# Performance work log

Hardware: AMD Instinct MI355X
Metric: run time of the kernel (lower is better)

The kernel has to match this reference:

```python
import jax, jax.numpy as jnp
import numpy as np


def setup_inputs() -> dict:
    key = jax.random.key(0)
    k1, k2, k3, k4 = jax.random.split(key, 4)
    N, E, DIN, DOUT = 16384, 8192, 128, 128
    x = jax.random.normal(k1, (N, DIN), dtype=jnp.float32)
    # sparse binary incidence matrix, avg node degree ~ E * 0.005 ~ 41
    H = (jax.random.uniform(k2, (N, E)) < 0.005).astype(jnp.float32)
    W = jax.random.normal(k3, (DOUT, DIN), dtype=jnp.float32) * (1.0 / np.sqrt(DIN))
    b = jax.random.normal(k4, (DOUT,), dtype=jnp.float32) * 0.01
    return {"x": x, "H": H, "W": W, "b": b}


def reference(x, H, W, b):
    # Degree vectors. Original builds dense diag matrices; off-diagonal zeros
    # raised to negative powers become inf and are zeroed by nan_to_num, so the
    # math reduces to elementwise inverse powers of the degree vectors with
    # non-finite entries mapped to 0.
    deg_node = jnp.sum(H, axis=1)                    # [N]
    deg_edge = jnp.sum(H, axis=0)                    # [E]
    dvih = jnp.where(deg_node > 0, deg_node ** -0.5, 0.0)   # D_v^{-1/2}
    dei = jnp.where(deg_edge > 0, 1.0 / deg_edge, 0.0)      # D_e^{-1}
    # D_v^{-1/2} H D_e^{-1} H^T D_v^{-1/2} x, as broadcasted row scalings
    y = dvih[:, None] * x                            # [N, DIN]
    y = H.T @ y                                      # [E, DIN]
    y = dei[:, None] * y                             # [E, DIN]
    y = H @ y                                        # [N, DIN]
    y = dvih[:, None] * y                            # [N, DIN]
    return y @ W.T + b                               # [N, DOUT]
```

## Files before the change

### kernel.cpp

```cpp
#include <hip/hip_runtime.h>
#include <hip/hip_bf16.h>

#define NN 16384
#define EE 8192
#define DD 128
#define CSR_STRIDE 128
#define CSC_STRIDE 192

typedef float vfloat4 __attribute__((ext_vector_type(4)));

__device__ __forceinline__ unsigned short f2bf(float f) {
    union { float f; unsigned u; } c; c.f = f;
    unsigned u = c.u + (0x7FFFu + ((c.u >> 16) & 1u));
    return (unsigned short)(u >> 16);
}
__device__ __forceinline__ float bf2f(unsigned short h) {
    union { unsigned u; float f; } c; c.u = ((unsigned)h) << 16;
    return c.f;
}


__global__ __launch_bounds__(256) void g_gemm(
    const float* __restrict__ x,
    const float* __restrict__ W,
    ushort4* __restrict__ xwb,
    int* __restrict__ edge_cnt)
{
    const int t = threadIdx.x;
    {
        int tid = blockIdx.x * 256 + t;
        if (tid < EE) edge_cnt[tid] = 0;
    }

    __shared__ float sA[32 * 132];
    __shared__ float sW[64 * 132];
    const int m0 = blockIdx.x * 32;

#pragma unroll
    for (int r = 0; r < 4; ++r) {
        int i = t + 256 * r;
        int row = i >> 5, c4 = (i & 31) << 2;
        *(float4*)&sA[row * 132 + c4] =
            *(const float4*)&x[(size_t)(m0 + row) * DD + c4];
    }

    const int jg = t & 15;
    const int mg = t >> 4;
    const int m2 = mg * 2;
    const int j4 = jg * 4;

    for (int h = 0; h < 2; ++h) {
        __syncthreads();
#pragma unroll
        for (int r = 0; r < 8; ++r) {
            int i = t + 256 * r;
            int row = i >> 5, c4 = (i & 31) << 2;
            *(float4*)&sW[row * 132 + c4] =
                *(const float4*)&W[(size_t)(h * 64 + row) * DD + c4];
        }
        __syncthreads();

        float acc0[4] = {0.f, 0.f, 0.f, 0.f};
        float acc1[4] = {0.f, 0.f, 0.f, 0.f};
#pragma unroll 4
        for (int k = 0; k < 128; k += 4) {
            float4 a0 = *(const float4*)&sA[m2 * 132 + k];
            float4 a1 = *(const float4*)&sA[(m2 + 1) * 132 + k];
#pragma unroll
            for (int jj = 0; jj < 4; ++jj) {
                float4 w = *(const float4*)&sW[(j4 + jj) * 132 + k];
                acc0[jj] += a0.x*w.x + a0.y*w.y + a0.z*w.z + a0.w*w.w;
                acc1[jj] += a1.x*w.x + a1.y*w.y + a1.z*w.z + a1.w*w.w;
            }
        }
        ushort4 p0, p1;
        p0.x = f2bf(acc0[0]); p0.y = f2bf(acc0[1]); p0.z = f2bf(acc0[2]); p0.w = f2bf(acc0[3]);
        p1.x = f2bf(acc1[0]); p1.y = f2bf(acc1[1]); p1.z = f2bf(acc1[2]); p1.w = f2bf(acc1[3]);
        xwb[(size_t)(m0 + m2)     * 32 + h * 16 + jg] = p0;
        xwb[(size_t)(m0 + m2 + 1) * 32 + h * 16 + jg] = p1;
    }
}

__global__ __launch_bounds__(256) void k1_parse(
    const float* __restrict__ H,
    float* __restrict__ dvih,
    int* __restrict__ csr_cnt,
    int* __restrict__ csr_idx,
    int* __restrict__ edge_cnt,
    int* __restrict__ csc_idx)
{
    const int n = blockIdx.x;
    const int t = threadIdx.x;
    __shared__ int s_cnt;
    __shared__ int s_list[CSR_STRIDE];
    if (t == 0) s_cnt = 0;
    __syncthreads();

    const vfloat4* row = (const vfloat4*)(H + (size_t)n * EE);
#pragma unroll
    for (int j = 0; j < 8; ++j) {
        int idx = t + 256 * j;
        vfloat4 v = __builtin_nontemporal_load(row + idx);
        int base = idx * 4;
        if (v[0] != 0.0f) { int p = atomicAdd(&s_cnt, 1); if (p < CSR_STRIDE) s_list[p] = base + 0; }
        if (v[1] != 0.0f) { int p = atomicAdd(&s_cnt, 1); if (p < CSR_STRIDE) s_list[p] = base + 1; }
        if (v[2] != 0.0f) { int p = atomicAdd(&s_cnt, 1); if (p < CSR_STRIDE) s_list[p] = base + 2; }
        if (v[3] != 0.0f) { int p = atomicAdd(&s_cnt, 1); if (p < CSR_STRIDE) s_list[p] = base + 3; }
    }
    __syncthreads();

    int cnt = s_cnt; if (cnt > CSR_STRIDE) cnt = CSR_STRIDE;
    if (t < cnt) {
        int e = s_list[t];
        csr_idx[(size_t)n * CSR_STRIDE + t] = e;
        int pos = atomicAdd(&edge_cnt[e], 1);
        if (pos < CSC_STRIDE) csc_idx[(size_t)e * CSC_STRIDE + pos] = n;
    }
    if (t == 0) {
        csr_cnt[n] = cnt;
        dvih[n] = (cnt > 0) ? (1.0f / sqrtf((float)cnt)) : 0.0f;
    }
}

__global__ __launch_bounds__(256) void k2_edge_gather(
    const ushort4* __restrict__ xwb,
    const float* __restrict__ dvih,
    const int* __restrict__ edge_cnt,
    const int* __restrict__ csc_idx,
    ushort4* __restrict__ y2b)
{
    const int t    = threadIdx.x;
    const int w    = t >> 6;
    const int lane = t & 63;
    const int grp  = lane >> 5;
    const int fl   = lane & 31;
    const int e    = blockIdx.x * 4 + w;

    __shared__ int    s_lst[4][CSC_STRIDE];
    __shared__ float  s_dv[4][CSC_STRIDE];

    int cnt = edge_cnt[e];
    int ccnt = cnt > CSC_STRIDE ? CSC_STRIDE : cnt;
    for (int i = lane; i < ccnt; i += 64) {
        int n = csc_idx[(size_t)e * CSC_STRIDE + i];
        s_lst[w][i] = n;
        s_dv[w][i]  = dvih[n];
    }
    __syncthreads();

    float ax = 0.f, ay = 0.f, az = 0.f, aw = 0.f;
    int i = grp;
    for (; i + 14 < ccnt; i += 16) {
        ushort4 v0 = xwb[(size_t)s_lst[w][i     ] * 32 + fl];
        ushort4 v1 = xwb[(size_t)s_lst[w][i +  2] * 32 + fl];
        ushort4 v2 = xwb[(size_t)s_lst[w][i +  4] * 32 + fl];
        ushort4 v3 = xwb[(size_t)s_lst[w][i +  6] * 32 + fl];
        ushort4 v4 = xwb[(size_t)s_lst[w][i +  8] * 32 + fl];
        ushort4 v5 = xwb[(size_t)s_lst[w][i + 10] * 32 + fl];
        ushort4 v6 = xwb[(size_t)s_lst[w][i + 12] * 32 + fl];
        ushort4 v7 = xwb[(size_t)s_lst[w][i + 14] * 32 + fl];
        float f0 = s_dv[w][i],      f1 = s_dv[w][i +  2];
        float f2 = s_dv[w][i +  4], f3 = s_dv[w][i +  6];
        float f4 = s_dv[w][i +  8], f5 = s_dv[w][i + 10];
        float f6 = s_dv[w][i + 12], f7 = s_dv[w][i + 14];
        ax += f0*bf2f(v0.x) + f1*bf2f(v1.x) + f2*bf2f(v2.x) + f3*bf2f(v3.x)
            + f4*bf2f(v4.x) + f5*bf2f(v5.x) + f6*bf2f(v6.x) + f7*bf2f(v7.x);
        ay += f0*bf2f(v0.y) + f1*bf2f(v1.y) + f2*bf2f(v2.y) + f3*bf2f(v3.y)
            + f4*bf2f(v4.y) + f5*bf2f(v5.y) + f6*bf2f(v6.y) + f7*bf2f(v7.y);
        az += f0*bf2f(v0.z) + f1*bf2f(v1.z) + f2*bf2f(v2.z) + f3*bf2f(v3.z)
            + f4*bf2f(v4.z) + f5*bf2f(v5.z) + f6*bf2f(v6.z) + f7*bf2f(v7.z);
        aw += f0*bf2f(v0.w) + f1*bf2f(v1.w) + f2*bf2f(v2.w) + f3*bf2f(v3.w)
            + f4*bf2f(v4.w) + f5*bf2f(v5.w) + f6*bf2f(v6.w) + f7*bf2f(v7.w);
    }
    for (; i < ccnt; i += 2) {
        ushort4 v = xwb[(size_t)s_lst[w][i] * 32 + fl];
        float f = s_dv[w][i];
        ax += f*bf2f(v.x); ay += f*bf2f(v.y); az += f*bf2f(v.z); aw += f*bf2f(v.w);
    }

    ax += __shfl_xor(ax, 32);
    ay += __shfl_xor(ay, 32);
    az += __shfl_xor(az, 32);
    aw += __shfl_xor(aw, 32);

    if (grp == 0) {
        float dei = (cnt > 0) ? (1.0f / (float)cnt) : 0.0f;
        ushort4 o;
        o.x = f2bf(ax * dei);
        o.y = f2bf(ay * dei);
        o.z = f2bf(az * dei);
        o.w = f2bf(aw * dei);
        y2b[(size_t)e * 32 + fl] = o;
    }
}

__global__ __launch_bounds__(256) void k3_node_gather(
    const ushort4* __restrict__ y2b,
    const float* __restrict__ dvih,
    const int* __restrict__ csr_cnt,
    const int* __restrict__ csr_idx,
    const float* __restrict__ b,
    float* __restrict__ out)
{
    const int t    = threadIdx.x;
    const int w    = t >> 6;
    const int lane = t & 63;
    const int grp  = lane >> 5;
    const int fl   = lane & 31;
    const int n    = blockIdx.x * 4 + w;

    __shared__ int s_lst[4][CSR_STRIDE];

    int cnt = csr_cnt[n];
    for (int i = lane; i < cnt; i += 64)
        s_lst[w][i] = csr_idx[(size_t)n * CSR_STRIDE + i];
    __syncthreads();

    float ax = 0.f, ay = 0.f, az = 0.f, aw = 0.f;
    int i = grp;
    for (; i + 6 < cnt; i += 8) {
        ushort4 v0 = y2b[(size_t)s_lst[w][i    ] * 32 + fl];
        ushort4 v1 = y2b[(size_t)s_lst[w][i + 2] * 32 + fl];
        ushort4 v2 = y2b[(size_t)s_lst[w][i + 4] * 32 + fl];
        ushort4 v3 = y2b[(size_t)s_lst[w][i + 6] * 32 + fl];
        ax += bf2f(v0.x) + bf2f(v1.x) + bf2f(v2.x) + bf2f(v3.x);
        ay += bf2f(v0.y) + bf2f(v1.y) + bf2f(v2.y) + bf2f(v3.y);
        az += bf2f(v0.z) + bf2f(v1.z) + bf2f(v2.z) + bf2f(v3.z);
        aw += bf2f(v0.w) + bf2f(v1.w) + bf2f(v2.w) + bf2f(v3.w);
    }
    for (; i < cnt; i += 2) {
        ushort4 v = y2b[(size_t)s_lst[w][i] * 32 + fl];
        ax += bf2f(v.x); ay += bf2f(v.y); az += bf2f(v.z); aw += bf2f(v.w);
    }

    ax += __shfl_xor(ax, 32);
    ay += __shfl_xor(ay, 32);
    az += __shfl_xor(az, 32);
    aw += __shfl_xor(aw, 32);

    if (grp == 0) {
        float dv = dvih[n];
        float4 bb = ((const float4*)b)[fl];
        float4 o = make_float4(ax * dv + bb.x,
                               ay * dv + bb.y,
                               az * dv + bb.z,
                               aw * dv + bb.w);
        ((float4*)out)[(size_t)n * 32 + fl] = o;
    }
}

extern "C" void kernel_launch(void* const* d_in, const int* in_sizes, int n_in,
                              void* d_out, int out_size, void* d_ws, size_t ws_size,
                              hipStream_t stream) {
    const float* x = (const float*)d_in[0];
    const float* H = (const float*)d_in[1];
    const float* W = (const float*)d_in[2];
    const float* b = (const float*)d_in[3];
    float* out = (float*)d_out;

    char* ws = (char*)d_ws;
    float*   dvih    = (float*)  (ws + 0);
    int*     csr_cnt = (int*)    (ws + 65536);
    int*     edge_cnt= (int*)    (ws + 131072);
    int*     csr_idx = (int*)    (ws + 163840);
    int*     csc_idx = (int*)    (ws + 8552448);
    ushort4* xwb     = (ushort4*)(ws + 14843904);
    ushort4* y2b     = (ushort4*)(ws + 19038208);

    g_gemm<<<NN / 32, 256, 0, stream>>>(x, W, xwb, edge_cnt);
    k1_parse<<<NN, 256, 0, stream>>>(H, dvih, csr_cnt, csr_idx, edge_cnt, csc_idx);
    k2_edge_gather<<<EE / 4, 256, 0, stream>>>(xwb, dvih, edge_cnt, csc_idx, y2b);
    k3_node_gather<<<NN / 4, 256, 0, stream>>>(y2b, dvih, csr_cnt, csr_idx, b, out);
}
```

Before: 729.9 us.

## Fuse GEMM and H-parse into one launch, move edge_cnt reset to memset

Merges the dense x·W^T GEMM and the H-row parse into a single kernel, with the first 512 blocks doing the GEMM and the rest parsing H rows, so the small GEMM overlaps with the bandwidth-bound H scan. The GEMM now reads x and W directly from global memory with no LDS staging. The edge_cnt zeroing moves to a hipMemsetAsync, and the index loads in the gather kernels become nontemporal. The trade-off is more global and L2 traffic in the GEMM blocks and an extra memset launch.

```diff
diff --git a/kernel.cpp b/kernel.cpp
--- a/kernel.cpp
+++ b/kernel.cpp
@@ -6,6 +6,7 @@
 #define DD 128
 #define CSR_STRIDE 128
 #define CSC_STRIDE 192
+#define GEMM_BLOCKS 512
 
 typedef float vfloat4 __attribute__((ext_vector_type(4)));
 
@@ -20,79 +21,55 @@
 }
 
 
-__global__ __launch_bounds__(256) void g_gemm(
+__global__ __launch_bounds__(256) void k01_fused(
     const float* __restrict__ x,
     const float* __restrict__ W,
+    const float* __restrict__ H,
     ushort4* __restrict__ xwb,
-    int* __restrict__ edge_cnt)
-{
-    const int t = threadIdx.x;
-    {
-        int tid = blockIdx.x * 256 + t;
-        if (tid < EE) edge_cnt[tid] = 0;
-    }
-
-    __shared__ float sA[32 * 132];
-    __shared__ float sW[64 * 132];
-    const int m0 = blockIdx.x * 32;
-
-#pragma unroll
-    for (int r = 0; r < 4; ++r) {
-        int i = t + 256 * r;
-        int row = i >> 5, c4 = (i & 31) << 2;
-        *(float4*)&sA[row * 132 + c4] =
-            *(const float4*)&x[(size_t)(m0 + row) * DD + c4];
-    }
-
-    const int jg = t & 15;
-    const int mg = t >> 4;
-    const int m2 = mg * 2;
-    const int j4 = jg * 4;
-
-    for (int h = 0; h < 2; ++h) {
-        __syncthreads();
-#pragma unroll
-        for (int r = 0; r < 8; ++r) {
-            int i = t + 256 * r;
-            int row = i >> 5, c4 = (i & 31) << 2;
-            *(float4*)&sW[row * 132 + c4] =
-                *(const float4*)&W[(size_t)(h * 64 + row) * DD + c4];
-        }
-        __syncthreads();
-
-        float acc0[4] = {0.f, 0.f, 0.f, 0.f};
-        float acc1[4] = {0.f, 0.f, 0.f, 0.f};
-#pragma unroll 4
-        for (int k = 0; k < 128; k += 4) {
-            float4 a0 = *(const float4*)&sA[m2 * 132 + k];
-            float4 a1 = *(const float4*)&sA[(m2 + 1) * 132 + k];
-#pragma unroll
-            for (int jj = 0; jj < 4; ++jj) {
-                float4 w = *(const float4*)&sW[(j4 + jj) * 132 + k];
-                acc0[jj] += a0.x*w.x + a0.y*w.y + a0.z*w.z + a0.w*w.w;
-                acc1[jj] += a1.x*w.x + a1.y*w.y + a1.z*w.z + a1.w*w.w;
-            }
-        }
-        ushort4 p0, p1;
-        p0.x = f2bf(acc0[0]); p0.y = f2bf(acc0[1]); p0.z = f2bf(acc0[2]); p0.w = f2bf(acc0[3]);
-        p1.x = f2bf(acc1[0]); p1.y = f2bf(acc1[1]); p1.z = f2bf(acc1[2]); p1.w = f2bf(acc1[3]);
-        xwb[(size_t)(m0 + m2)     * 32 + h * 16 + jg] = p0;
-        xwb[(size_t)(m0 + m2 + 1) * 32 + h * 16 + jg] = p1;
-    }
-}
-
-__global__ __launch_bounds__(256) void k1_parse(
-    const float* __restrict__ H,
     float* __restrict__ dvih,
     int* __restrict__ csr_cnt,
     int* __restrict__ csr_idx,
     int* __restrict__ edge_cnt,
     int* __restrict__ csc_idx)
 {
-    const int n = blockIdx.x;
     const int t = threadIdx.x;
     __shared__ int s_cnt;
     __shared__ int s_list[CSR_STRIDE];
+
+    if (blockIdx.x < GEMM_BLOCKS) {
+        const int m0 = blockIdx.x * 32;
+        const int jg = t & 15;
+        const int mg = t >> 4;
+        const int m2 = mg * 2;
+        const int j4 = jg * 4;
+        const float* a0p = x + (size_t)(m0 + m2) * DD;
+        const float* a1p = a0p + DD;
+
+        for (int h = 0; h < 2; ++h) {
+            const float* wb = W + (size_t)(h * 64 + j4) * DD;
+            float acc0[4] = {0.f, 0.f, 0.f, 0.f};
+            float acc1[4] = {0.f, 0.f, 0.f, 0.f};
+#pragma unroll 4
+            for (int k = 0; k < 128; k += 4) {
+                float4 a0 = *(const float4*)&a0p[k];
+                float4 a1 = *(const float4*)&a1p[k];
+#pragma unroll
+                for (int jj = 0; jj < 4; ++jj) {
+                    float4 w = *(const float4*)&wb[jj * DD + k];
+                    acc0[jj] += a0.x*w.x + a0.y*w.y + a0.z*w.z + a0.w*w.w;
+                    acc1[jj] += a1.x*w.x + a1.y*w.y + a1.z*w.z + a1.w*w.w;
+                }
+            }
+            ushort4 p0, p1;
+            p0.x = f2bf(acc0[0]); p0.y = f2bf(acc0[1]); p0.z = f2bf(acc0[2]); p0.w = f2bf(acc0[3]);
+            p1.x = f2bf(acc1[0]); p1.y = f2bf(acc1[1]); p1.z = f2bf(acc1[2]); p1.w = f2bf(acc1[3]);
+            xwb[(size_t)(m0 + m2)     * 32 + h * 16 + jg] = p0;
+            xwb[(size_t)(m0 + m2 + 1) * 32 + h * 16 + jg] = p1;
+        }
+        return;
+    }
+
+    const int n = blockIdx.x - GEMM_BLOCKS;
     if (t == 0) s_cnt = 0;
     __syncthreads();
 
@@ -142,7 +119,7 @@
     int cnt = edge_cnt[e];
     int ccnt = cnt > CSC_STRIDE ? CSC_STRIDE : cnt;
     for (int i = lane; i < ccnt; i += 64) {
-        int n = csc_idx[(size_t)e * CSC_STRIDE + i];
+        int n = __builtin_nontemporal_load(&csc_idx[(size_t)e * CSC_STRIDE + i]);
         s_lst[w][i] = n;
         s_dv[w][i]  = dvih[n];
     }
@@ -213,7 +190,7 @@
 
     int cnt = csr_cnt[n];
     for (int i = lane; i < cnt; i += 64)
-        s_lst[w][i] = csr_idx[(size_t)n * CSR_STRIDE + i];
+        s_lst[w][i] = __builtin_nontemporal_load(&csr_idx[(size_t)n * CSR_STRIDE + i]);
     __syncthreads();
 
     float ax = 0.f, ay = 0.f, az = 0.f, aw = 0.f;
@@ -267,8 +244,9 @@
     ushort4* xwb     = (ushort4*)(ws + 14843904);
     ushort4* y2b     = (ushort4*)(ws + 19038208);
 
-    g_gemm<<<NN / 32, 256, 0, stream>>>(x, W, xwb, edge_cnt);
-    k1_parse<<<NN, 256, 0, stream>>>(H, dvih, csr_cnt, csr_idx, edge_cnt, csc_idx);
+    hipMemsetAsync(edge_cnt, 0, EE * sizeof(int), stream);
+    k01_fused<<<GEMM_BLOCKS + NN, 256, 0, stream>>>(
+        x, W, H, xwb, dvih, csr_cnt, csr_idx, edge_cnt, csc_idx);
     k2_edge_gather<<<EE / 4, 256, 0, stream>>>(xwb, dvih, edge_cnt, csc_idx, y2b);
     k3_node_gather<<<NN / 4, 256, 0, stream>>>(y2b, dvih, csr_cnt, csr_idx, b, out);
 }
```

Measured after the change: 797.1 us. 9.2% more time.
